# Kernel optimization log

Hardware: AMD Instinct MI355X
Metric: run time of the kernel (lower is better)

## Reference

```python
import jax, jax.numpy as jnp
import numpy as np

B, C, H, W = 2048, 4, 64, 64
K = 3  # shift / patch kernel size


def _l2_normalize(x, axis=-1, eps=1e-12):
    n = jnp.linalg.norm(x, axis=axis, keepdims=True)
    return x / jnp.maximum(n, eps)


def _circular_convolution(weights, kernel):
    # weights: [B,H,W], kernel: [B,3,3] (softmax-normalized shift kernel)
    res = jnp.zeros_like(weights)
    c = K // 2
    for dh in range(K):
        for dw in range(K):
            coeff = kernel[:, dh, dw][:, None, None]
            res = res + coeff * jnp.roll(weights, shift=(dh - c, dw - c), axis=(1, 2))
    return res


def _apply_patch(weights, patch):
    # weights: [B,H,W], patch: [B,C,3,3] -> [B,C,H,W]; zero-padded (non-circular) shifts
    c = K // 2
    wp = jnp.pad(weights, ((0, 0), (c, c), (c, c)))  # [B,H+2,W+2]
    res = jnp.zeros((weights.shape[0], patch.shape[1], H, W), dtype=weights.dtype)
    for dh in range(K):
        for dw in range(K):
            coeff = patch[:, :, dh, dw][:, :, None, None]  # [B,C,1,1]
            # result[y,x] += patch[dh,dw] * weights[y-(dh-c), x-(dw-c)] within bounds
            win = wp[:, 2 * c - dh:2 * c - dh + H, 2 * c - dw:2 * c - dw + W]  # [B,H,W]
            res = res + coeff * win[:, None, :, :]
    return res


def setup_inputs() -> dict:
    key = jax.random.key(0)
    ks = jax.random.split(key, 12)
    return {
        "map_state": jax.random.uniform(ks[0], (B, C, H, W), dtype=jnp.float32),
        "weight_state": jnp.ones((B, H, W), dtype=jnp.float32) / float(H * W),
        "key": jax.random.normal(ks[1], (B, C), dtype=jnp.float32),
        "beta": jax.random.normal(ks[2], (B, 1), dtype=jnp.float32),
        "gate": jax.random.normal(ks[3], (B, 1), dtype=jnp.float32),
        "shift": jax.random.normal(ks[4], (B, K * K), dtype=jnp.float32),
        "sharpen": jax.random.normal(ks[5], (B, 1), dtype=jnp.float32),
        "erase": jax.random.normal(ks[6], (B, C), dtype=jnp.float32),
        "add": jax.random.normal(ks[7], (B, C), dtype=jnp.float32),
        "add_patch_logits": jax.random.normal(ks[8], (B, C, K, K), dtype=jnp.float32),
        "erase_patch_logits": jax.random.normal(ks[9], (B, C, K, K), dtype=jnp.float32),
    }


def reference(map_state, weight_state, key, beta, gate, shift, sharpen, erase, add,
              add_patch_logits, erase_patch_logits):
    b = map_state.shape[0]
    # content addressing: cosine similarity against flattened memory
    flat_mem = map_state.reshape(b, C, H * W).transpose(0, 2, 1)  # [B,HW,C]
    key_norm = _l2_normalize(key)                                  # [B,C]
    mem_norm = _l2_normalize(flat_mem)                             # [B,HW,C]
    similarity = jnp.einsum('bnc,bc->bn', mem_norm, key_norm)      # [B,HW]
    beta_pos = jax.nn.softplus(beta) + 1e-6                        # [B,1]
    content_w = jax.nn.softmax(beta_pos * similarity, axis=-1)
    # interpolation gate with previous weights
    gate_sigma = jax.nn.sigmoid(gate)                              # [B,1]
    prev_w = weight_state.reshape(b, -1)
    gated = gate_sigma * content_w + (1.0 - gate_sigma) * prev_w
    # differentiable circular shift
    shift_kernel = jax.nn.softmax(shift, axis=-1).reshape(b, K, K)
    shifted = _circular_convolution(gated.reshape(b, H, W), shift_kernel)
    # sharpening
    sharpen_pos = 1.0 + jax.nn.softplus(sharpen)                   # [B,1]
    sharpened = jnp.clip(shifted, 1e-6, None).reshape(b, -1) ** sharpen_pos
    weights = sharpened / (jnp.sum(sharpened, axis=-1, keepdims=True) + 1e-6)
    weights = weights / (jnp.sum(weights, axis=-1, keepdims=True) + 1e-6)
    weights_2d = weights.reshape(b, H, W)
    # patch-based write (add + erase)
    add_patch = jax.nn.sigmoid(add_patch_logits)
    erase_patch = jax.nn.sigmoid(erase_patch_logits)
    add_map = _apply_patch(weights_2d, add_patch)
    erase_map = jnp.clip(_apply_patch(weights_2d, erase_patch), 0.0, 1.0)
    map_updated = map_state * (1.0 - erase_map) + add_map
    read_vector = jnp.sum(map_updated * weights_2d[:, None, :, :], axis=(2, 3))  # [B,C]
    return map_updated, weights_2d, read_vector
```

## Files before the change

### kernel.cpp

```cpp
#include <hip/hip_runtime.h>
#include <math.h>

#define CC 4
#define HH 64
#define WW 64
#define NN (HH*WW)
#define NTH 256
#define GRP 4
#define LDW 65

typedef float vf4 __attribute__((ext_vector_type(4)));

#if __has_builtin(__builtin_amdgcn_exp2f)
#define FEXP2(x) __builtin_amdgcn_exp2f(x)
#else
#define FEXP2(x) exp2f(x)
#endif
#if __has_builtin(__builtin_amdgcn_logf)
#define FLOG2(x) __builtin_amdgcn_logf(x)
#else
#define FLOG2(x) log2f(x)
#endif
#define LOG2E 1.4426950408889634f

__device__ __forceinline__ float softplusf(float x) {
    return (x > 20.f) ? x : log1pf(expf(x));
}
__device__ __forceinline__ float sigmoidf(float x) {
    return 1.f / (1.f + expf(-x));
}

__device__ __forceinline__ float bred(float v, float* sc, bool do_max) {
#pragma unroll
    for (int o = 32; o > 0; o >>= 1) {
        float other = __shfl_down(v, o, 64);
        v = do_max ? fmaxf(v, other) : (v + other);
    }
    if ((threadIdx.x & 63) == 0) sc[threadIdx.x >> 6] = v;
    __syncthreads();
    return do_max ? fmaxf(fmaxf(sc[0], sc[1]), fmaxf(sc[2], sc[3]))
                  : ((sc[0] + sc[1]) + (sc[2] + sc[3]));
}

__global__ __launch_bounds__(NTH)
void slam_kernel(const float* __restrict__ map_state,
                 const float* __restrict__ weight_state,
                 const float* __restrict__ key,
                 const float* __restrict__ beta,
                 const float* __restrict__ gate,
                 const float* __restrict__ shift,
                 const float* __restrict__ sharpen,
                 const float* __restrict__ add_patch_logits,
                 const float* __restrict__ erase_patch_logits,
                 float* __restrict__ out_map,
                 float* __restrict__ out_w,
                 float* __restrict__ out_rv)
{
    __shared__ float sw[HH * LDW];
    __shared__ float spatch[2 * CC * 9];
    __shared__ float sks[9];
    __shared__ float sred[8][4];

    const int b = blockIdx.x;
    const int tid = threadIdx.x;

    const float* keyb = key + b * CC;
    float k0 = keyb[0], k1 = keyb[1], k2 = keyb[2], k3 = keyb[3];
    {
        float inv = rsqrtf(fmaxf(k0*k0 + k1*k1 + k2*k2 + k3*k3, 1e-24f));
        k0 *= inv; k1 *= inv; k2 *= inv; k3 *= inv;
    }
    const float beta_pos  = softplusf(beta[b]) + 1e-6f;
    const float g         = sigmoidf(gate[b]);
    const float sharp_pos = 1.f + softplusf(sharpen[b]);

    if (tid == 0) {
        const float* sh = shift + b * 9;
        float m = sh[0];
#pragma unroll
        for (int i = 1; i < 9; ++i) m = fmaxf(m, sh[i]);
        float s = 0.f;
        float e[9];
#pragma unroll
        for (int i = 0; i < 9; ++i) { e[i] = FEXP2((sh[i] - m) * LOG2E); s += e[i]; }
        float inv = 1.f / s;
#pragma unroll
        for (int i = 0; i < 9; ++i) sks[i] = e[i] * inv;
    }

    if (tid < 2 * CC * 9) {
        float v = (tid < CC * 9) ? add_patch_logits[b * CC * 9 + tid]
                                 : erase_patch_logits[b * CC * 9 + (tid - CC * 9)];
        spatch[tid] = sigmoidf(v);
    }

    const vf4* mp4 = (const vf4*)(map_state    + (size_t)b * CC * NN);
    const vf4* pw4 = (const vf4*)(weight_state + (size_t)b * NN);
    vf4*       om4 = (vf4*)(out_map + (size_t)b * CC * NN);
    vf4*       ow4 = (vf4*)(out_w   + (size_t)b * NN);

    float z[16];

    float lmax = -INFINITY;
#pragma unroll 1
    for (int gix = 0; gix < GRP; ++gix) {
        const int base = tid + gix * NTH;
        vf4 mv0 = mp4[base];
        vf4 mv1 = mp4[(NN/4) + base];
        vf4 mv2 = mp4[2*(NN/4) + base];
        vf4 mv3 = mp4[3*(NN/4) + base];
#pragma unroll
        for (int j = 0; j < 4; ++j) {
            float a0 = mv0[j];
            float a1 = mv1[j];
            float a2 = mv2[j];
            float a3 = mv3[j];
            float inv = rsqrtf(fmaxf(a0*a0 + a1*a1 + a2*a2 + a3*a3, 1e-24f));
            float zz = beta_pos * (a0*k0 + a1*k1 + a2*k2 + a3*k3) * inv;
            z[gix*4 + j] = zz;
            lmax = fmaxf(lmax, zz);
        }
    }
    const float zmax = bred(lmax, sred[0], true);

    float lsum = 0.f;
#pragma unroll
    for (int i = 0; i < 16; ++i) {
        float e = FEXP2((z[i] - zmax) * LOG2E);
        z[i] = e;
        lsum += e;
    }
    const float Z = bred(lsum, sred[1], false);
    const float gZinv = g / Z;
    const float g1 = 1.f - g;

#pragma unroll
    for (int gix = 0; gix < GRP; ++gix) {
        const int base = tid + gix * NTH;
        const int P = 4 * base, h = P >> 6, w0 = P & 63;
        vf4 pw = __builtin_nontemporal_load(&pw4[base]);
        float* row = sw + h * LDW + w0;
#pragma unroll
        for (int j = 0; j < 4; ++j)
            row[j] = gZinv * z[gix*4 + j] + g1 * pw[j];
    }
    __syncthreads();

    float lsum1 = 0.f;
#pragma unroll
    for (int gix = 0; gix < GRP; ++gix) {
        const int P = 4 * (tid + gix * NTH), h = P >> 6, w0 = P & 63;
        const int rr[3] = { (h + 1) & 63, h, (h + 63) & 63 };
        const int cm = (w0 + 63) & 63, cp = (w0 + 4) & 63;
        float acc0 = 0.f, acc1 = 0.f, acc2 = 0.f, acc3 = 0.f;
#pragma unroll
        for (int dh = 0; dh < 3; ++dh) {
            const float* rp = sw + rr[dh] * LDW;
            float b0 = rp[cm];
            float b1 = rp[w0];
            float b2 = rp[w0 + 1];
            float b3 = rp[w0 + 2];
            float b4 = rp[w0 + 3];
            float b5 = rp[cp];
            float s0 = sks[dh*3+0], s1 = sks[dh*3+1], s2 = sks[dh*3+2];
            acc0 += s0*b2 + s1*b1 + s2*b0;
            acc1 += s0*b3 + s1*b2 + s2*b1;
            acc2 += s0*b4 + s1*b3 + s2*b2;
            acc3 += s0*b5 + s1*b4 + s2*b3;
        }
        float p0 = FEXP2(sharp_pos * FLOG2(fmaxf(acc0, 1e-6f)));
        float p1 = FEXP2(sharp_pos * FLOG2(fmaxf(acc1, 1e-6f)));
        float p2 = FEXP2(sharp_pos * FLOG2(fmaxf(acc2, 1e-6f)));
        float p3 = FEXP2(sharp_pos * FLOG2(fmaxf(acc3, 1e-6f)));
        z[gix*4+0] = p0; z[gix*4+1] = p1; z[gix*4+2] = p2; z[gix*4+3] = p3;
        lsum1 += (p0 + p1) + (p2 + p3);
    }
    const float S1 = bred(lsum1, sred[2], false);
    const float inv1 = 1.f / (S1 + 1e-6f);
    const float S2 = S1 * inv1;
    const float scale = inv1 / (S2 + 1e-6f);

#pragma unroll
    for (int gix = 0; gix < GRP; ++gix) {
        const int base = tid + gix * NTH;
        const int P = 4 * base, h = P >> 6, w0 = P & 63;
        float* row = sw + h * LDW + w0;
        vf4 o;
#pragma unroll
        for (int j = 0; j < 4; ++j) {
            float wv = z[gix*4 + j] * scale;
            row[j] = wv;
            o[j] = wv;
        }
        __builtin_nontemporal_store(o, &ow4[base]);
    }
    __syncthreads();

    float rv[CC] = {0.f, 0.f, 0.f, 0.f};
#pragma unroll 1
    for (int gix = 0; gix < GRP; ++gix) {
        const int base = tid + gix * NTH;
        const int P = 4 * base, h = P >> 6, w0 = P & 63;
        float buf[3][6];
#pragma unroll
        for (int dh = 0; dh < 3; ++dh) {
            const int r = h + 1 - dh;
            if ((unsigned)r < (unsigned)HH) {
                const float* rp = sw + r * LDW;
                buf[dh][0] = (w0 > 0) ? rp[w0 - 1] : 0.f;
                buf[dh][1] = rp[w0];
                buf[dh][2] = rp[w0 + 1];
                buf[dh][3] = rp[w0 + 2];
                buf[dh][4] = rp[w0 + 3];
                buf[dh][5] = (w0 + 4 < WW) ? rp[w0 + 4] : 0.f;
            } else {
#pragma unroll
                for (int k = 0; k < 6; ++k) buf[dh][k] = 0.f;
            }
        }
        const float wn0 = buf[1][1], wn1 = buf[1][2], wn2 = buf[1][3], wn3 = buf[1][4];
#pragma unroll
        for (int ch = 0; ch < CC; ++ch) {
            vf4 m4 = __builtin_nontemporal_load(&mp4[ch * (NN/4) + base]);
            float a0 = 0.f, a1 = 0.f, a2 = 0.f, a3 = 0.f;
            float e0 = 0.f, e1 = 0.f, e2 = 0.f, e3 = 0.f;
#pragma unroll
            for (int dh = 0; dh < 3; ++dh) {
#pragma unroll
                for (int t = 0; t < 3; ++t) {
                    const float ca = spatch[ch * 9 + dh * 3 + t];
                    const float ce = spatch[CC * 9 + ch * 9 + dh * 3 + t];
                    a0 += ca * buf[dh][2 - t];  e0 += ce * buf[dh][2 - t];
                    a1 += ca * buf[dh][3 - t];  e1 += ce * buf[dh][3 - t];
                    a2 += ca * buf[dh][4 - t];  e2 += ce * buf[dh][4 - t];
                    a3 += ca * buf[dh][5 - t];  e3 += ce * buf[dh][5 - t];
                }
            }
            vf4 o;
            float mu;
            mu = m4[0] * (1.f - fminf(fmaxf(e0, 0.f), 1.f)) + a0;
            o[0] = mu; rv[ch] += mu * wn0;
            mu = m4[1] * (1.f - fminf(fmaxf(e1, 0.f), 1.f)) + a1;
            o[1] = mu; rv[ch] += mu * wn1;
            mu = m4[2] * (1.f - fminf(fmaxf(e2, 0.f), 1.f)) + a2;
            o[2] = mu; rv[ch] += mu * wn2;
            mu = m4[3] * (1.f - fminf(fmaxf(e3, 0.f), 1.f)) + a3;
            o[3] = mu; rv[ch] += mu * wn3;
            __builtin_nontemporal_store(o, &om4[ch * (NN/4) + base]);
        }
    }

#pragma unroll
    for (int c = 0; c < CC; ++c) {
        float v = rv[c];
#pragma unroll
        for (int o = 32; o > 0; o >>= 1) v += __shfl_down(v, o, 64);
        if ((tid & 63) == 0) sred[4 + c][tid >> 6] = v;
    }
    __syncthreads();
    if (tid == 0) {
#pragma unroll
        for (int c = 0; c < CC; ++c)
            out_rv[(size_t)b * CC + c] =
                (sred[4+c][0] + sred[4+c][1]) + (sred[4+c][2] + sred[4+c][3]);
    }
}

extern "C" void kernel_launch(void* const* d_in, const int* in_sizes, int n_in,
                              void* d_out, int out_size, void* d_ws, size_t ws_size,
                              hipStream_t stream) {
    const float* map_state          = (const float*)d_in[0];
    const float* weight_state       = (const float*)d_in[1];
    const float* key                = (const float*)d_in[2];
    const float* beta               = (const float*)d_in[3];
    const float* gate               = (const float*)d_in[4];
    const float* shift              = (const float*)d_in[5];
    const float* sharpen            = (const float*)d_in[6];
    const float* add_patch_logits   = (const float*)d_in[9];
    const float* erase_patch_logits = (const float*)d_in[10];

    const int B = in_sizes[1] / NN;

    float* out_map = (float*)d_out;
    float* out_w   = out_map + (size_t)B * CC * NN;
    float* out_rv  = out_w   + (size_t)B * NN;

    slam_kernel<<<B, NTH, 0, stream>>>(map_state, weight_state, key, beta, gate,
                                       shift, sharpen, add_patch_logits,
                                       erase_patch_logits, out_map, out_w, out_rv);
}
```

Baseline: 78.37 us.

## Split fused kernel into separate weights and apply kernels

Splits the single per-batch kernel into two launches. The first computes the addressing weights and writes them to global memory. The second re-reads map_state and the weights, then applies the patch write and the read. This likely lowers register and shared-memory pressure per kernel, which could raise occupancy. In exchange it re-reads map_state (128 MB) and the weights from global memory, which adds substantial extra traffic to a memory-bound workload.

```diff
diff --git a/kernel.cpp b/kernel.cpp
--- a/kernel.cpp
+++ b/kernel.cpp
@@ -43,23 +43,18 @@
 }
 
 __global__ __launch_bounds__(NTH)
-void slam_kernel(const float* __restrict__ map_state,
-                 const float* __restrict__ weight_state,
-                 const float* __restrict__ key,
-                 const float* __restrict__ beta,
-                 const float* __restrict__ gate,
-                 const float* __restrict__ shift,
-                 const float* __restrict__ sharpen,
-                 const float* __restrict__ add_patch_logits,
-                 const float* __restrict__ erase_patch_logits,
-                 float* __restrict__ out_map,
-                 float* __restrict__ out_w,
-                 float* __restrict__ out_rv)
+void weights_kernel(const float* __restrict__ map_state,
+                    const float* __restrict__ weight_state,
+                    const float* __restrict__ key,
+                    const float* __restrict__ beta,
+                    const float* __restrict__ gate,
+                    const float* __restrict__ shift,
+                    const float* __restrict__ sharpen,
+                    float* __restrict__ out_w)
 {
     __shared__ float sw[HH * LDW];
-    __shared__ float spatch[2 * CC * 9];
     __shared__ float sks[9];
-    __shared__ float sred[8][4];
+    __shared__ float sred[4][4];
 
     const int b = blockIdx.x;
     const int tid = threadIdx.x;
@@ -88,16 +83,9 @@
         for (int i = 0; i < 9; ++i) sks[i] = e[i] * inv;
     }
 
-    if (tid < 2 * CC * 9) {
-        float v = (tid < CC * 9) ? add_patch_logits[b * CC * 9 + tid]
-                                 : erase_patch_logits[b * CC * 9 + (tid - CC * 9)];
-        spatch[tid] = sigmoidf(v);
-    }
-
     const vf4* mp4 = (const vf4*)(map_state    + (size_t)b * CC * NN);
     const vf4* pw4 = (const vf4*)(weight_state + (size_t)b * NN);
-    vf4*       om4 = (vf4*)(out_map + (size_t)b * CC * NN);
-    vf4*       ow4 = (vf4*)(out_w   + (size_t)b * NN);
+    vf4*       ow4 = (vf4*)(out_w + (size_t)b * NN);
 
     float z[16];
 
@@ -111,10 +99,7 @@
         vf4 mv3 = mp4[3*(NN/4) + base];
 #pragma unroll
         for (int j = 0; j < 4; ++j) {
-            float a0 = mv0[j];
-            float a1 = mv1[j];
-            float a2 = mv2[j];
-            float a3 = mv3[j];
+            float a0 = mv0[j], a1 = mv1[j], a2 = mv2[j], a3 = mv3[j];
             float inv = rsqrtf(fmaxf(a0*a0 + a1*a1 + a2*a2 + a3*a3, 1e-24f));
             float zz = beta_pos * (a0*k0 + a1*k1 + a2*k2 + a3*k3) * inv;
             z[gix*4 + j] = zz;
@@ -156,12 +141,8 @@
 #pragma unroll
         for (int dh = 0; dh < 3; ++dh) {
             const float* rp = sw + rr[dh] * LDW;
-            float b0 = rp[cm];
-            float b1 = rp[w0];
-            float b2 = rp[w0 + 1];
-            float b3 = rp[w0 + 2];
-            float b4 = rp[w0 + 3];
-            float b5 = rp[cp];
+            float b0 = rp[cm], b1 = rp[w0], b2 = rp[w0+1];
+            float b3 = rp[w0+2], b4 = rp[w0+3], b5 = rp[cp];
             float s0 = sks[dh*3+0], s1 = sks[dh*3+1], s2 = sks[dh*3+2];
             acc0 += s0*b2 + s1*b1 + s2*b0;
             acc1 += s0*b3 + s1*b2 + s2*b1;
@@ -183,16 +164,46 @@
 #pragma unroll
     for (int gix = 0; gix < GRP; ++gix) {
         const int base = tid + gix * NTH;
+        vf4 o;
+#pragma unroll
+        for (int j = 0; j < 4; ++j) o[j] = z[gix*4 + j] * scale;
+        ow4[base] = o;
+    }
+}
+
+__global__ __launch_bounds__(NTH)
+void apply_kernel(const float* __restrict__ map_state,
+                  const float* __restrict__ add_patch_logits,
+                  const float* __restrict__ erase_patch_logits,
+                  const float* __restrict__ w_in,
+                  float* __restrict__ out_map,
+                  float* __restrict__ out_rv)
+{
+    __shared__ float sw[HH * LDW];
+    __shared__ float spatch[2 * CC * 9];
+    __shared__ float sred[4][4];
+
+    const int b = blockIdx.x;
+    const int tid = threadIdx.x;
+
+    if (tid < 2 * CC * 9) {
+        float v = (tid < CC * 9) ? add_patch_logits[b * CC * 9 + tid]
+                                 : erase_patch_logits[b * CC * 9 + (tid - CC * 9)];
+        spatch[tid] = sigmoidf(v);
+    }
+
+    const vf4* mp4 = (const vf4*)(map_state + (size_t)b * CC * NN);
+    const vf4* w4  = (const vf4*)(w_in      + (size_t)b * NN);
+    vf4*       om4 = (vf4*)(out_map + (size_t)b * CC * NN);
+
+#pragma unroll
+    for (int gix = 0; gix < GRP; ++gix) {
+        const int base = tid + gix * NTH;
         const int P = 4 * base, h = P >> 6, w0 = P & 63;
+        vf4 wv = w4[base];
         float* row = sw + h * LDW + w0;
-        vf4 o;
-#pragma unroll
-        for (int j = 0; j < 4; ++j) {
-            float wv = z[gix*4 + j] * scale;
-            row[j] = wv;
-            o[j] = wv;
-        }
-        __builtin_nontemporal_store(o, &ow4[base]);
+#pragma unroll
+        for (int j = 0; j < 4; ++j) row[j] = wv[j];
     }
     __syncthreads();
 
@@ -255,14 +266,14 @@
         float v = rv[c];
 #pragma unroll
         for (int o = 32; o > 0; o >>= 1) v += __shfl_down(v, o, 64);
-        if ((tid & 63) == 0) sred[4 + c][tid >> 6] = v;
+        if ((tid & 63) == 0) sred[c][tid >> 6] = v;
     }
     __syncthreads();
     if (tid == 0) {
 #pragma unroll
         for (int c = 0; c < CC; ++c)
             out_rv[(size_t)b * CC + c] =
-                (sred[4+c][0] + sred[4+c][1]) + (sred[4+c][2] + sred[4+c][3]);
+                (sred[c][0] + sred[c][1]) + (sred[c][2] + sred[c][3]);
     }
 }
 
@@ -285,7 +296,9 @@
     float* out_w   = out_map + (size_t)B * CC * NN;
     float* out_rv  = out_w   + (size_t)B * NN;
 
-    slam_kernel<<<B, NTH, 0, stream>>>(map_state, weight_state, key, beta, gate,
-                                       shift, sharpen, add_patch_logits,
-                                       erase_patch_logits, out_map, out_w, out_rv);
-}
+    weights_kernel<<<B, NTH, 0, stream>>>(map_state, weight_state, key, beta,
+                                          gate, shift, sharpen, out_w);
+    apply_kernel<<<B, NTH, 0, stream>>>(map_state, add_patch_logits,
+                                        erase_patch_logits, out_w,
+                                        out_map, out_rv);
+}
```

New measurement: 88.05 us. +12.3%, slower.
